# Optimization experiments

Hardware: AMD Instinct MI355X
Metric: run time of the kernel (lower is better)

The kernel has to match this reference:

```python
import jax, jax.numpy as jnp
import numpy as np

TEMP = 10.0
BPE = 4
BER = 0.01
K = 2 ** BPE  # number of centers


def setup_inputs() -> dict:
    key = jax.random.key(0)
    k1, k2 = jax.random.split(key)
    x = jax.random.normal(k1, (32, 256, 32, 32), dtype=jnp.float32)
    center = jax.random.normal(k2, (K,), dtype=jnp.float32)
    return {"x": x, "center": center}


def reference(x, center):
    # Q_type == 'Soft' path of quantizer_channel.forward
    # residuals to every center: [B, C, H, W, K]
    d = x[..., None] - center
    # nearest-center index (hard assignment)
    W_index = jnp.argmin(jnp.abs(d), axis=-1)  # int32 [B,C,H,W]
    # soft assignment and soft quantized value
    smx = jax.nn.softmax(-TEMP * (d * d), axis=-1)
    W_soft = jnp.einsum('bchwk,k->bchw', smx, center)
    # bitmap rows are the binary expansion of the index, MSB first;
    # map[W_index][..., j] == (W_index >> (BPE-1-j)) & 1
    shifts = jnp.arange(BPE - 1, -1, -1, dtype=jnp.int32)  # [BPE]
    bits = (W_index[..., None] >> shifts) & 1  # [B,C,H,W,BPE]
    # bernoulli bit-flip channel noise; (bit + noise) % 2 == XOR
    noise = jax.random.bernoulli(jax.random.key(42), BER, bits.shape).astype(bits.dtype)
    noisy_bits = bits ^ noise
    # index = sum_i 2^i * bits[..., BPE-1-i]  ==  dot with 2^shifts
    idx_noisy = jnp.sum(noisy_bits * (2 ** shifts), axis=-1)
    W_noisy = center[idx_noisy]
    # soft value with stop-gradient channel bias (straight-through noise)
    return W_soft + jax.lax.stop_gradient(W_noisy - W_soft)
```

## Files before the change

### kernel.cpp

```cpp
#include <hip/hip_runtime.h>
#include <stdint.h>


#define KS1 42u
#define KS2 0x1BD11BF0u
#define BERN_LT 42950144u

__device__ __forceinline__ uint32_t rotl(uint32_t x, int r) {
  return __builtin_amdgcn_alignbit(x, x, (32 - r) & 31);
}

#define TF_ROUND4(r)                                            \
  { _Pragma("unroll") for (int j = 0; j < 4; ++j) {             \
      y0[j] += y1[j];                                           \
      y1[j] = rotl(y1[j], (r)) ^ y0[j];                         \
  } }

#define TF_INJ4(a, b)                                           \
  { _Pragma("unroll") for (int j = 0; j < 4; ++j) {             \
      y0[j] += (a); y1[j] += (b);                               \
  } }

__global__ __launch_bounds__(256) void quantizer_channel_kernel(
    const float* __restrict__ x, const float* __restrict__ center,
    float* __restrict__ out, int n4)
{
  int t = blockIdx.x * blockDim.x + threadIdx.x;
  if (t >= n4) return;

  float c[16];
#pragma unroll
  for (int k = 0; k < 16; ++k) c[k] = center[k];

  const float4 xv = reinterpret_cast<const float4*>(x)[t];
  float xe[4] = {xv.x, xv.y, xv.z, xv.w};
  float oe[4];

  const uint32_t ctr_base = (uint32_t)t * 16u;

#pragma unroll
  for (int e = 0; e < 4; ++e) {
    const float v = xe[e];
    float bd = fabsf(v - c[0]);
    int best = 0;
#pragma unroll
    for (int k = 1; k < 16; ++k) {
      const float d = fabsf(v - c[k]);
      best = (d < bd) ? k : best;
      bd = fminf(d, bd);
    }

    uint32_t y0[4], y1[4];
#pragma unroll
    for (int j = 0; j < 4; ++j) {
      y0[j] = 0u;
      y1[j] = (ctr_base + 4u * (uint32_t)e + (uint32_t)j) + KS1;
    }
    TF_ROUND4(13) TF_ROUND4(15) TF_ROUND4(26) TF_ROUND4(6)
    TF_INJ4(KS1, KS2 + 1u)
    TF_ROUND4(17) TF_ROUND4(29) TF_ROUND4(16) TF_ROUND4(24)
    TF_INJ4(KS2, 0u + 2u)
    TF_ROUND4(13) TF_ROUND4(15) TF_ROUND4(26) TF_ROUND4(6)
    TF_INJ4(0u, KS1 + 3u)
    TF_ROUND4(17) TF_ROUND4(29) TF_ROUND4(16) TF_ROUND4(24)
    TF_INJ4(KS1, KS2 + 4u)
    TF_ROUND4(13) TF_ROUND4(15) TF_ROUND4(26) TF_ROUND4(6)
    TF_INJ4(KS2, 0u + 5u)

    uint32_t flip = 0u;
#pragma unroll
    for (int j = 0; j < 4; ++j) {
      const uint32_t bits = y0[j] ^ y1[j];
      const uint32_t hit = (bits < BERN_LT) ? 1u : 0u;
      flip |= hit << (3 - j);
    }

    oe[e] = center[(uint32_t)best ^ flip];
  }

  float4 o4;
  o4.x = oe[0]; o4.y = oe[1]; o4.z = oe[2]; o4.w = oe[3];
  reinterpret_cast<float4*>(out)[t] = o4;
}

extern "C" void kernel_launch(void* const* d_in, const int* in_sizes, int n_in,
                              void* d_out, int out_size, void* d_ws, size_t ws_size,
                              hipStream_t stream)
{
  const float* x      = (const float*)d_in[0];
  const float* center = (const float*)d_in[1];
  float* out          = (float*)d_out;

  const int N  = in_sizes[0];
  const int n4 = N / 4;
  const int block = 256;
  const int grid  = (n4 + block - 1) / block;

  hipLaunchKernelGGL(quantizer_channel_kernel, dim3(grid), dim3(block), 0, stream,
                     x, center, out, n4);
}
```

Before: 75.63 us.

## Replace linear nearest-center scan with sorted-threshold binary search

Adds a small setup kernel that sorts the 16 centers and computes exact float decision boundaries between neighbouring centers, plus a packed rank-to-index lookup table. The main kernel then finds the nearest center with a 4-level branchless binary search over these thresholds instead of 16 abs/compare/select steps per element. This cuts ALU work in the argmin, but the Threefry RNG still dominates per-element compute, and the extra kernel launch adds serial overhead.

```diff
diff --git a/kernel.cpp b/kernel.cpp
--- a/kernel.cpp
+++ b/kernel.cpp
@@ -6,16 +6,64 @@
 #define KS2 0x1BD11BF0u
 #define BERN_LT 42950144u
 
+__device__ __forceinline__ uint32_t fkey(float f) {
+  uint32_t u = __float_as_uint(f);
+  return (u & 0x80000000u) ? ~u : (u | 0x80000000u);
+}
+__device__ __forceinline__ float finv(uint32_t k) {
+  uint32_t u = (k & 0x80000000u) ? (k & 0x7fffffffu) : ~k;
+  return __uint_as_float(u);
+}
+
+__global__ void quantizer_setup_kernel(const float* __restrict__ center,
+                                       float* __restrict__ ws) {
+  const int t = threadIdx.x;
+  __shared__ float sval[16];
+  __shared__ int   sidx[16];
+  if (t < 16) {
+    const float ct = center[t];
+    int rank = 0;
+    for (int j = 0; j < 16; ++j) {
+      const float cj = center[j];
+      rank += (cj < ct || (cj == ct && j < t)) ? 1 : 0;
+    }
+    sval[rank] = ct;
+    sidx[rank] = t;
+  }
+  __syncthreads();
+  if (t < 15) {
+    const float sL = sval[t], sR = sval[t + 1];
+    const bool tieLeft = sidx[t] < sidx[t + 1];
+    uint32_t lo = fkey(sL), hi = fkey(sR);
+    while (hi - lo > 1u) {
+      const uint32_t mid = lo + ((hi - lo) >> 1);
+      const float xm = finv(mid);
+      const float dL = fabsf(xm - sL);
+      const float dR = fabsf(xm - sR);
+      const bool left = (dL < dR) || (dL == dR && tieLeft);
+      if (left) lo = mid; else hi = mid;
+    }
+    ws[t] = finv(lo);
+  }
+  if (t == 15) {
+    uint32_t l0 = 0, l1 = 0;
+    for (int p = 0; p < 8; ++p) l0 |= ((uint32_t)sidx[p])     << (4 * p);
+    for (int p = 0; p < 8; ++p) l1 |= ((uint32_t)sidx[p + 8]) << (4 * p);
+    uint32_t* wu = (uint32_t*)ws;
+    wu[15] = 0u;
+    wu[16] = l0;
+    wu[17] = l1;
+  }
+}
+
 __device__ __forceinline__ uint32_t rotl(uint32_t x, int r) {
   return __builtin_amdgcn_alignbit(x, x, (32 - r) & 31);
 }
-
 #define TF_ROUND4(r)                                            \
   { _Pragma("unroll") for (int j = 0; j < 4; ++j) {             \
       y0[j] += y1[j];                                           \
       y1[j] = rotl(y1[j], (r)) ^ y0[j];                         \
   } }
-
 #define TF_INJ4(a, b)                                           \
   { _Pragma("unroll") for (int j = 0; j < 4; ++j) {             \
       y0[j] += (a); y1[j] += (b);                               \
@@ -23,14 +71,19 @@
 
 __global__ __launch_bounds__(256) void quantizer_channel_kernel(
     const float* __restrict__ x, const float* __restrict__ center,
-    float* __restrict__ out, int n4)
+    const float* __restrict__ ws, float* __restrict__ out, int n4)
 {
-  int t = blockIdx.x * blockDim.x + threadIdx.x;
+  const int t = blockIdx.x * blockDim.x + threadIdx.x;
   if (t >= n4) return;
 
-  float c[16];
-#pragma unroll
-  for (int k = 0; k < 16; ++k) c[k] = center[k];
+  const float4* wsf = (const float4*)ws;
+  const float4 ta = wsf[0], tb = wsf[1], tc = wsf[2], td = wsf[3];
+  const float T0 = ta.x, T1 = ta.y, T2  = ta.z, T3  = ta.w;
+  const float T4 = tb.x, T5 = tb.y, T6  = tb.z, T7  = tb.w;
+  const float T8 = tc.x, T9 = tc.y, T10 = tc.z, T11 = tc.w;
+  const float T12 = td.x, T13 = td.y, T14 = td.z;
+  const uint32_t lut0 = ((const uint32_t*)ws)[16];
+  const uint32_t lut1 = ((const uint32_t*)ws)[17];
 
   const float4 xv = reinterpret_cast<const float4*>(x)[t];
   float xe[4] = {xv.x, xv.y, xv.z, xv.w};
@@ -41,14 +94,21 @@
 #pragma unroll
   for (int e = 0; e < 4; ++e) {
     const float v = xe[e];
-    float bd = fabsf(v - c[0]);
-    int best = 0;
-#pragma unroll
-    for (int k = 1; k < 16; ++k) {
-      const float d = fabsf(v - c[k]);
-      best = (d < bd) ? k : best;
-      bd = fminf(d, bd);
-    }
+
+    const bool b3 = v > T7;
+    const float s2 = b3 ? T11 : T3;
+    const bool b2 = v > s2;
+    const float s1 = b3 ? (b2 ? T13 : T9) : (b2 ? T5 : T1);
+    const bool b1 = v > s1;
+    const float u0 = b1 ? T2  : T0;
+    const float u1 = b1 ? T6  : T4;
+    const float u2 = b1 ? T10 : T8;
+    const float u3 = b1 ? T14 : T12;
+    const float s0 = b3 ? (b2 ? u3 : u2) : (b2 ? u1 : u0);
+    const bool b0 = v > s0;
+    const uint32_t shamt = (b2 ? 16u : 0u) | (b1 ? 8u : 0u) | (b0 ? 4u : 0u);
+    const uint32_t word = b3 ? lut1 : lut0;
+    const uint32_t best = (word >> shamt) & 15u;
 
     uint32_t y0[4], y1[4];
 #pragma unroll
@@ -75,7 +135,7 @@
       flip |= hit << (3 - j);
     }
 
-    oe[e] = center[(uint32_t)best ^ flip];
+    oe[e] = center[best ^ flip];
   }
 
   float4 o4;
@@ -90,6 +150,10 @@
   const float* x      = (const float*)d_in[0];
   const float* center = (const float*)d_in[1];
   float* out          = (float*)d_out;
+  float* ws           = (float*)d_ws;
+
+  hipLaunchKernelGGL(quantizer_setup_kernel, dim3(1), dim3(64), 0, stream,
+                     center, ws);
 
   const int N  = in_sizes[0];
   const int n4 = N / 4;
@@ -97,5 +161,5 @@
   const int grid  = (n4 + block - 1) / block;
 
   hipLaunchKernelGGL(quantizer_channel_kernel, dim3(grid), dim3(block), 0, stream,
-                     x, center, out, n4);
+                     x, center, ws, out, n4);
 }
```

Result: no change. 74.43 us (-1.6%).
